# Performance work log

Hardware: AMD Instinct MI355X
Metric: run time of the kernel (lower is better)

The kernel has to match this reference:

```python
import jax, jax.numpy as jnp
import numpy as np

N_ROLES = 6
EPS = 1e-5

def _ln(x, scale, bias):
    m = jnp.mean(x, axis=-1, keepdims=True)
    v = jnp.var(x, axis=-1, keepdims=True)
    return (x - m) * jax.lax.rsqrt(v + EPS) * scale + bias

def setup_inputs() -> dict:
    key = jax.random.key(0)
    ks = jax.random.split(key, 20)
    T, B, D_OBS, H, A = 32, 1024, 256, 512, 32
    inp = {
        'rnn_states': jax.random.normal(ks[0], (B, H), jnp.float32),
        'obs': jax.random.normal(ks[1], (T, B, D_OBS), jnp.float32),
        'resets': jnp.zeros((T, B), jnp.float32),
        'available_actions': jnp.ones((T, B, A), jnp.float32),
        'role_ids': jax.random.randint(ks[2], (T, B), 0, N_ROLES, jnp.int32),
        # feature norm over obs_dim
        'fn_scale': jnp.ones((D_OBS,), jnp.float32),
        'fn_bias': jnp.zeros((D_OBS,), jnp.float32),
        # base MLP: obs_dim->512->512, each followed by LayerNorm
        'W0': jax.random.normal(ks[3], (D_OBS, H), jnp.float32) * 0.02,
        'b0': jnp.zeros((H,), jnp.float32),
        'ln0_scale': jnp.ones((H,), jnp.float32),
        'ln0_bias': jnp.zeros((H,), jnp.float32),
        'W1': jax.random.normal(ks[4], (H, H), jnp.float32) * 0.02,
        'b1': jnp.zeros((H,), jnp.float32),
        'ln1_scale': jnp.ones((H,), jnp.float32),
        'ln1_bias': jnp.zeros((H,), jnp.float32),
        # per-role routes: obs_dim->128->H (stacked over roles)
        'Wr0': jax.random.normal(ks[5], (N_ROLES, D_OBS, 128), jnp.float32) * 0.02,
        'br0': jnp.zeros((N_ROLES, 128), jnp.float32),
        'Wr1': jax.random.normal(ks[6], (N_ROLES, 128, H), jnp.float32) * 0.02,
        'br1': jnp.zeros((N_ROLES, H), jnp.float32),
        # per-role heads: H->64->32->action_dim (stacked over roles)
        'Wh0': jax.random.normal(ks[7], (N_ROLES, H, 64), jnp.float32) * 0.02,
        'bh0': jnp.zeros((N_ROLES, 64), jnp.float32),
        'Wh1': jax.random.normal(ks[8], (N_ROLES, 64, 32), jnp.float32) * 0.02,
        'bh1': jnp.zeros((N_ROLES, 32), jnp.float32),
        'Wh2': jax.random.normal(ks[9], (N_ROLES, 32, A), jnp.float32) * 0.02,
        'bh2': jnp.zeros((N_ROLES, A), jnp.float32),
    }
    return inp

def _gather_by_role(all_values, role_ids):
    # all_values: (K, T, B, F); role_ids: (T, B) -> (T, B, F)
    idx = role_ids[None, :, :, None].astype(jnp.int32)
    return jnp.take_along_axis(all_values, idx, axis=0)[0]

def reference(rnn_states, obs, resets, available_actions, role_ids,
              fn_scale, fn_bias, W0, b0, ln0_scale, ln0_bias,
              W1, b1, ln1_scale, ln1_bias,
              Wr0, br0, Wr1, br1,
              Wh0, bh0, Wh1, bh1, Wh2, bh2):
    # feature normalization on raw obs
    obs_n = _ln(obs, fn_scale, fn_bias)
    # shared base MLP (relu + LayerNorm after each Dense)
    e = _ln(jax.nn.relu(obs_n @ W0 + b0), ln0_scale, ln0_bias)
    e = _ln(jax.nn.relu(e @ W1 + b1), ln1_scale, ln1_bias)
    # per-role pre-GRU residual routes on (normalized) obs
    r = jax.nn.relu(jnp.einsum('tbi,kih->ktbh', obs_n, Wr0) + br0[:, None, None, :])
    r = jax.nn.relu(jnp.einsum('ktbh,kho->ktbo', r, Wr1) + br1[:, None, None, :])
    e = e + _gather_by_role(r, role_ids)
    # no recurrent policy configured: rnn_states pass through
    # per-role heads -> all logits (K, T, B, A)
    h = jax.nn.relu(jnp.einsum('tbh,khf->ktbf', e, Wh0) + bh0[:, None, None, :])
    h = jax.nn.relu(jnp.einsum('ktbf,kfg->ktbg', h, Wh1) + bh1[:, None, None, :])
    all_logits = jnp.einsum('ktbg,kga->ktba', h, Wh2) + bh2[:, None, None, :]
    logits = _gather_by_role(all_logits, role_ids)
    logits = jnp.where(available_actions > 0.5, logits, jnp.full_like(logits, -1e10))
    return rnn_states, logits
```

## Files before the change

### kernel.cpp

```cpp
#include <hip/hip_runtime.h>
#include <stdint.h>

typedef unsigned short u16;
typedef unsigned int u32;

using bf16x8 = __attribute__((ext_vector_type(8))) short;
using f32x4  = __attribute__((ext_vector_type(4))) float;

#define DEVINL __device__ __forceinline__

DEVINL float b2f(u16 u) { return __builtin_bit_cast(float, (u32)u << 16); }
DEVINL u16 f2b(float f) {
  u32 u = __builtin_bit_cast(u32, f);
  u += 0x7FFFu + ((u >> 16) & 1u);
  return (u16)(u >> 16);
}

DEVINL void gll16(const u16* src, u16* dst) {
  __builtin_amdgcn_global_load_lds(
      (const __attribute__((address_space(1))) void*)(uintptr_t)src,
      (__attribute__((address_space(3))) void*)(uintptr_t)dst, 16, 0, 0);
}

#define MFMA __builtin_amdgcn_mfma_f32_16x16x32_bf16
#define NROLE 6

DEVINL void tp_tile(const float* __restrict__ s, u16* __restrict__ d,
                    int R, int C, int bx, int by, int z)
{
  __shared__ u16 tile[32][33];
  const size_t mstride = (size_t)R * C;
  s += (size_t)z * mstride;
  d += (size_t)z * mstride;
  int r0 = bx * 32, c0 = by * 32;
  int tx = threadIdx.x & 31, ty = threadIdx.x >> 5;
#pragma unroll
  for (int i = 0; i < 32; i += 8)
    tile[ty + i][tx] = f2b(s[(size_t)(r0 + ty + i) * C + (c0 + tx)]);
  __syncthreads();
#pragma unroll
  for (int i = 0; i < 32; i += 8)
    d[(size_t)(c0 + ty + i) * R + (r0 + tx)] = tile[tx][ty + i];
}

__global__ __launch_bounds__(256) void mega0(
    const float* W0, const float* W1, const float* Wr0, const float* Wr1, const float* Wh0,
    u16* W0t, u16* W1t, u16* Wr0t, u16* Wr1t, u16* Wh0t,
    const int* __restrict__ rid, int* __restrict__ blkCnt,
    const float* __restrict__ rnn, float* __restrict__ outRnn)
{
  int b = blockIdx.x;
  const int tid = threadIdx.x;
  if (b < 1152) {
    if (b < 128)      {            tp_tile(W0, W0t, 256, 512, b % 8,  b / 8, 0); }
    else if (b < 384) { b -= 128;  tp_tile(W1, W1t, 512, 512, b % 16, b / 16, 0); }
    else if (b < 576) { b -= 384;  int t = b / 8;  tp_tile(Wr0, Wr0t, 256, 128, b % 8,  t % 4,  t / 4); }
    else if (b < 960) { b -= 576;  int t = b / 4;  tp_tile(Wr1, Wr1t, 128, 512, b % 4,  t % 16, t / 16); }
    else              { b -= 960;  int t = b / 16; tp_tile(Wh0, Wh0t, 512, 64,  b % 16, t % 2,  t / 2); }
  } else if (b < 1280) {
    b -= 1152;
    __shared__ int h[NROLE];
    if (tid < NROLE) h[tid] = 0;
    __syncthreads();
    atomicAdd(&h[rid[b * 256 + tid]], 1);
    __syncthreads();
    if (tid < NROLE) blkCnt[b * NROLE + tid] = h[tid];
  } else {
    b -= 1280;
    const float4* src = (const float4*)rnn;
    float4* dst = (float4*)outRnn;
    int base = (b * 256 + tid) * 4;
#pragma unroll
    for (int i = 0; i < 4; ++i) dst[base + i] = src[base + i];
  }
}

__global__ __launch_bounds__(256, 2) void g0f(
    const float* __restrict__ obs, const float* __restrict__ fn_s,
    const float* __restrict__ fn_b, const u16* __restrict__ W0t,
    const float* __restrict__ b0, const float* __restrict__ ln0sc,
    const float* __restrict__ ln0bi, u16* __restrict__ obs_n,
    u16* __restrict__ C,
    const int* __restrict__ rid, const int* __restrict__ blkCnt,
    int* __restrict__ bucket, int* __restrict__ baseArr, int* __restrict__ cntArr)
{
  __shared__ __align__(16) u16 smem[20480];
  const int tid = threadIdx.x;

  if (blockIdx.x >= 512) {
    const int bx = blockIdx.x - 512;
    int* c = (int*)smem;
    int* preArr = c + 768;
    int* scnt   = c + 776;
    int* sbase  = c + 784;
    int* h      = c + 792;
    for (int i = tid; i < 128 * NROLE; i += 256) c[i] = blkCnt[i];
    if (tid < NROLE) h[tid] = 0;
    __syncthreads();
    if (tid < NROLE) {
      int k = tid, run = 0, pre = 0;
      for (int b = 0; b < 128; ++b) { if (b == bx) pre = run; run += c[b * NROLE + k]; }
      scnt[k] = run; preArr[k] = pre;
    }
    __syncthreads();
    if (tid == 0) {
      int r = 0;
      for (int k = 0; k < NROLE; ++k) { sbase[k] = r; r += scnt[k]; }
    }
    __syncthreads();
    if (bx == 0 && tid < NROLE) { baseArr[tid] = sbase[tid]; cntArr[tid] = scnt[tid]; }
    int i = bx * 256 + tid;
    int k = rid[i];
    int pos = atomicAdd(&h[k], 1);
    bucket[sbase[k] + preArr[k] + pos] = i;
    return;
  }

  u16* smA     = smem;
  float* redS  = (float*)&smem[16384];
  float* redSS = (float*)&smem[16896];
  float* prm   = (float*)&smem[17408];
  const int rowBase = blockIdx.x * 64;
  const int lane = tid & 63, wave = tid >> 6;
  const int quad = lane >> 4, lm = lane & 15, l7 = lm & 7;

#pragma unroll
  for (int i = tid; i < 512; i += 256) {
    prm[i] = b0[i]; prm[512 + i] = ln0sc[i]; prm[1024 + i] = ln0bi[i];
  }

  {
    const int r = tid >> 2, q = tid & 3;
    const float* xr = obs + (size_t)(rowBase + r) * 256 + q * 64;
    float x[64];
#pragma unroll
    for (int jj = 0; jj < 16; ++jj)
      *(float4*)&x[jj * 4] = *(const float4*)(xr + jj * 4);
    float s = 0.f, s2 = 0.f;
#pragma unroll
    for (int p = 0; p < 64; ++p) { s += x[p]; s2 += x[p] * x[p]; }
    s  += __shfl_xor(s, 1, 64);  s  += __shfl_xor(s, 2, 64);
    s2 += __shfl_xor(s2, 1, 64); s2 += __shfl_xor(s2, 2, 64);
    float m = s * (1.f / 256.f);
    float var = s2 * (1.f / 256.f) - m * m;
    float inv = rsqrtf(var + 1e-5f);
    const float* fs = fn_s + q * 64;
    const float* fb = fn_b + q * 64;
    u16* og = obs_n + (size_t)(rowBase + r) * 256 + q * 64;
#pragma unroll
    for (int j = 0; j < 8; ++j) {
      float4 fs0 = *(const float4*)(fs + j * 8);
      float4 fs1 = *(const float4*)(fs + j * 8 + 4);
      float4 fb0 = *(const float4*)(fb + j * 8);
      float4 fb1 = *(const float4*)(fb + j * 8 + 4);
      u16 yy[8] __attribute__((aligned(16)));
      yy[0] = f2b((x[j*8+0] - m) * inv * fs0.x + fb0.x);
      yy[1] = f2b((x[j*8+1] - m) * inv * fs0.y + fb0.y);
      yy[2] = f2b((x[j*8+2] - m) * inv * fs0.z + fb0.z);
      yy[3] = f2b((x[j*8+3] - m) * inv * fs0.w + fb0.w);
      yy[4] = f2b((x[j*8+4] - m) * inv * fs1.x + fb1.x);
      yy[5] = f2b((x[j*8+5] - m) * inv * fs1.y + fb1.y);
      yy[6] = f2b((x[j*8+6] - m) * inv * fs1.z + fb1.z);
      yy[7] = f2b((x[j*8+7] - m) * inv * fs1.w + fb1.w);
      int cch = q * 8 + j;
      *(uint4*)&smA[r * 256 + ((cch ^ (r & 7)) * 8)] = *(uint4*)yy;
      *(uint4*)(og + j * 8) = *(uint4*)yy;
    }
  }

  const int wn = wave * 128;
  u32 bOff[8];
#pragma unroll
  for (int j = 0; j < 8; ++j)
    bOff[j] = (u32)(wn + j * 16 + lm) * 256u + (u32)(quad * 8);
  f32x4 acc[4][8] = {};
  bf16x8 bR[2][8];
#pragma unroll
  for (int p = 0; p < 2; ++p)
#pragma unroll
    for (int j = 0; j < 8; ++j)
      bR[p][j] = *(const bf16x8*)(W0t + bOff[j] + p * 32);
  __syncthreads();

#pragma unroll
  for (int g = 0; g < 8; ++g) {
    bf16x8 cur[8];
#pragma unroll
    for (int j = 0; j < 8; ++j) cur[j] = bR[g & 1][j];
    if (g + 2 < 8) {
#pragma unroll
      for (int j = 0; j < 8; ++j)
        bR[g & 1][j] = *(const bf16x8*)(W0t + bOff[j] + (g + 2) * 32);
    }
    const int kc = g * 4;
    bf16x8 af[4];
#pragma unroll
    for (int i2 = 0; i2 < 4; ++i2)
      af[i2] = *(const bf16x8*)&smA[(i2 * 16 + lm) * 256 + (((quad + kc) ^ l7) * 8)];
#pragma unroll
    for (int i2 = 0; i2 < 4; ++i2)
#pragma unroll
      for (int j = 0; j < 8; ++j)
        acc[i2][j] = MFMA(af[i2], cur[j], acc[i2][j], 0, 0, 0);
  }

#pragma unroll
  for (int i2 = 0; i2 < 4; ++i2) {
#pragma unroll
    for (int r2 = 0; r2 < 4; ++r2) {
      float s = 0.f, ss = 0.f;
#pragma unroll
      for (int j = 0; j < 8; ++j) {
        float v = fmaxf(acc[i2][j][r2] + prm[wn + j * 16 + lm], 0.f);
        acc[i2][j][r2] = v;
        s += v; ss += v * v;
      }
#pragma unroll
      for (int o = 1; o < 16; o <<= 1) { s += __shfl_xor(s, o, 64); ss += __shfl_xor(ss, o, 64); }
      if (lm == 0) {
        int rowL = i2 * 16 + quad * 4 + r2;
        redS[rowL * 4 + wave] = s;
        redSS[rowL * 4 + wave] = ss;
      }
    }
  }
  __syncthreads();
#pragma unroll
  for (int i2 = 0; i2 < 4; ++i2) {
#pragma unroll
    for (int r2 = 0; r2 < 4; ++r2) {
      int rowL = i2 * 16 + quad * 4 + r2;
      float ts  = redS[rowL * 4 + 0] + redS[rowL * 4 + 1] + redS[rowL * 4 + 2] + redS[rowL * 4 + 3];
      float tss = redSS[rowL * 4 + 0] + redSS[rowL * 4 + 1] + redSS[rowL * 4 + 2] + redSS[rowL * 4 + 3];
      float m = ts * (1.f / 512.f);
      float var = tss * (1.f / 512.f) - m * m;
      float inv = rsqrtf(var + 1e-5f);
      size_t base = (size_t)(rowBase + rowL) * 512;
#pragma unroll
      for (int j = 0; j < 8; ++j) {
        int col = wn + j * 16 + lm;
        float y = (acc[i2][j][r2] - m) * inv * prm[512 + col] + prm[1024 + col];
        C[base + col] = f2b(y);
      }
    }
  }
}

template <int K>
__global__ __launch_bounds__(256, 2) void gemm_ln(
    const u16* __restrict__ A, const u16* __restrict__ Bt,
    const float* __restrict__ bias, const float* __restrict__ lnsc,
    const float* __restrict__ lnbi, u16* __restrict__ C)
{
  constexpr int BK = 128, NI = K / BK, NC = K / 32;
  __shared__ __align__(16) u16 As[2][64 * BK];
  __shared__ float redS[64][4];
  __shared__ float redSS[64][4];
  __shared__ float prm[1536];
  const int tid = threadIdx.x;
  const int rowBase = blockIdx.x * 64;
  const int lane = tid & 63, wave = tid >> 6;
#pragma unroll
  for (int i = tid; i < 512; i += 256) {
    prm[i] = bias[i]; prm[512 + i] = lnsc[i]; prm[1024 + i] = lnbi[i];
  }
  u32 aOff[4];
#pragma unroll
  for (int r = 0; r < 4; ++r) {
    int row = r * 16 + (tid >> 4);
    int chunk = tid & 15;
    aOff[r] = (u32)(rowBase + row) * (u32)K + (u32)((chunk ^ (row & 7)) * 8);
  }
  const int quad = lane >> 4, lm = lane & 15, l7 = lm & 7;
  const int wn = wave * 128;
  u32 bOff[8];
#pragma unroll
  for (int j = 0; j < 8; ++j)
    bOff[j] = (u32)(wn + j * 16 + lm) * (u32)K + (u32)(quad * 8);

  f32x4 acc[4][8] = {};

#pragma unroll
  for (int r = 0; r < 4; ++r)
    gll16(A + aOff[r], &As[0][r * 2048 + wave * 512]);
  bf16x8 bP[8];
#pragma unroll
  for (int j = 0; j < 8; ++j)
    bP[j] = *(const bf16x8*)(Bt + bOff[j]);
  __syncthreads();

  for (int i = 0; i < NI; ++i) {
    const u16* Ab = As[i & 1];
    if (i + 1 < NI) {
#pragma unroll
      for (int r = 0; r < 4; ++r)
        gll16(A + aOff[r] + (i + 1) * BK, &As[(i + 1) & 1][r * 2048 + wave * 512]);
    }
#pragma unroll
    for (int c = 0; c < 4; ++c) {
      const int g = i * 4 + c;
      bf16x8 bN[8];
      if (g + 1 < NC) {
#pragma unroll
        for (int j = 0; j < 8; ++j)
          bN[j] = *(const bf16x8*)(Bt + bOff[j] + (g + 1) * 32);
      }
      const int kc = c * 4;
      bf16x8 af[4];
#pragma unroll
      for (int i2 = 0; i2 < 4; ++i2)
        af[i2] = *(const bf16x8*)&Ab[(i2 * 16 + lm) * BK + (((quad + kc) ^ l7) * 8)];
#pragma unroll
      for (int i2 = 0; i2 < 4; ++i2)
#pragma unroll
        for (int j = 0; j < 8; ++j)
          acc[i2][j] = MFMA(af[i2], bP[j], acc[i2][j], 0, 0, 0);
      if (g + 1 < NC) {
#pragma unroll
        for (int j = 0; j < 8; ++j) bP[j] = bN[j];
      }
    }
    __syncthreads();
  }

#pragma unroll
  for (int i2 = 0; i2 < 4; ++i2) {
#pragma unroll
    for (int r2 = 0; r2 < 4; ++r2) {
      float s = 0.f, ss = 0.f;
#pragma unroll
      for (int j = 0; j < 8; ++j) {
        float v = fmaxf(acc[i2][j][r2] + prm[wn + j * 16 + lm], 0.f);
        acc[i2][j][r2] = v;
        s += v; ss += v * v;
      }
#pragma unroll
      for (int o = 1; o < 16; o <<= 1) { s += __shfl_xor(s, o, 64); ss += __shfl_xor(ss, o, 64); }
      if (lm == 0) {
        int rowL = i2 * 16 + quad * 4 + r2;
        redS[rowL][wave] = s;
        redSS[rowL][wave] = ss;
      }
    }
  }
  __syncthreads();
#pragma unroll
  for (int i2 = 0; i2 < 4; ++i2) {
#pragma unroll
    for (int r2 = 0; r2 < 4; ++r2) {
      int rowL = i2 * 16 + quad * 4 + r2;
      float ts  = redS[rowL][0] + redS[rowL][1] + redS[rowL][2] + redS[rowL][3];
      float tss = redSS[rowL][0] + redSS[rowL][1] + redSS[rowL][2] + redSS[rowL][3];
      float m = ts * (1.f / 512.f);
      float var = tss * (1.f / 512.f) - m * m;
      float inv = rsqrtf(var + 1e-5f);
      size_t base = (size_t)(rowBase + rowL) * 512;
#pragma unroll
      for (int j = 0; j < 8; ++j) {
        int col = wn + j * 16 + lm;
        float y = (acc[i2][j][r2] - m) * inv * prm[512 + col] + prm[1024 + col];
        C[base + col] = f2b(y);
      }
    }
  }
}

__global__ __launch_bounds__(256, 4) void route_head(
    const u16* __restrict__ obs_n, const u16* __restrict__ e,
    const u16* __restrict__ Wr0t, const float* __restrict__ br0,
    const u16* __restrict__ Wr1t, const float* __restrict__ br1,
    const u16* __restrict__ Wh0t, const float* __restrict__ bh0,
    const float* __restrict__ Wh1, const float* __restrict__ bh1,
    const float* __restrict__ Wh2, const float* __restrict__ bh2,
    const float* __restrict__ avail,
    const int* __restrict__ bucket, const int* __restrict__ baseArr,
    const int* __restrict__ cntArr, float* __restrict__ outLogits)
{
  __shared__ __align__(16) u16 sm[20480];
  const int tid = threadIdx.x;

  int cA0, cA1, cA2, cA3, cA4, cA5, bA0, bA1, bA2, bA3, bA4, bA5;
  {
    int4 ca = *(const int4*)cntArr;  int2 cb = *(const int2*)(cntArr + 4);
    int4 ba = *(const int4*)baseArr; int2 bb = *(const int2*)(baseArr + 4);
    cA0 = ca.x; cA1 = ca.y; cA2 = ca.z; cA3 = ca.w; cA4 = cb.x; cA5 = cb.y;
    bA0 = ba.x; bA1 = ba.y; bA2 = ba.z; bA3 = ba.w; bA4 = bb.x; bA5 = bb.y;
  }
  int role = -1, rem = blockIdx.x, cnt = 0, roleBase = 0;
#define TRY_ROLE(k, ck, bk)                                        \
  if (role < 0) {                                                  \
    int tiles = ((ck) + 31) >> 5;                                  \
    if (rem < tiles) { role = (k); cnt = (ck); roleBase = (bk); }  \
    else rem -= tiles;                                             \
  }
  TRY_ROLE(0, cA0, bA0) TRY_ROLE(1, cA1, bA1) TRY_ROLE(2, cA2, bA2)
  TRY_ROLE(3, cA3, bA3) TRY_ROLE(4, cA4, bA4) TRY_ROLE(5, cA5, bA5)
#undef TRY_ROLE
  if (role < 0) return;
  const int limit = cnt;
  const int rowBase = rem * 32;

  const int lane = tid & 63, wave = tid >> 6;
  const int quad = lane >> 4, lm = lane & 15, l7 = lm & 7;

#pragma unroll
  for (int r = 0; r < 8; ++r) {
    int lrow = r * 4 + wave;
    int i = rowBase + lrow;
    if (i >= limit) i = rowBase;
    int grow = bucket[roleBase + i];
    int chunk = tid & 63;
    int sw = (chunk & 56) | ((chunk ^ lrow) & 7);
    gll16(e + (u32)grow * 512u + (u32)(sw * 8), &sm[r * 2048 + wave * 512]);
  }

  int growA0, growA1;
  {
    int i0 = rowBase + lm;        if (i0 >= limit) i0 = rowBase;
    int i1 = rowBase + 16 + lm;   if (i1 >= limit) i1 = rowBase;
    growA0 = bucket[roleBase + i0];
    growA1 = bucket[roleBase + i1];
  }
  const u16* Ag0 = obs_n + (size_t)growA0 * 256;
  const u16* Ag1 = obs_n + (size_t)growA1 * 256;

  const int wn0 = wave * 32;
  const u16* B0 = Wr0t + (size_t)role * 128 * 256;
  f32x4 acc0[2][2] = {};
  bf16x8 b0R[2][2];
#pragma unroll
  for (int p = 0; p < 2; ++p)
#pragma unroll
    for (int j = 0; j < 2; ++j)
      b0R[p][j] = *(const bf16x8*)(B0 + (u32)(wn0 + j * 16 + lm) * 256u + (u32)(quad * 8 + p * 32));
  bf16x8 aR[4][2];
#pragma unroll
  for (int p = 0; p < 4; ++p) {
    aR[p][0] = *(const bf16x8*)(Ag0 + (u32)(quad * 8 + p * 32));
    aR[p][1] = *(const bf16x8*)(Ag1 + (u32)(quad * 8 + p * 32));
  }
  float bias0[2] = { br0[role * 128 + wn0 + lm], br0[role * 128 + wn0 + 16 + lm] };
#pragma unroll
  for (int it = 0; it < 8; ++it) {
    bf16x8 a0 = aR[it & 3][0], a1 = aR[it & 3][1];
    bf16x8 cur0 = b0R[it & 1][0], cur1 = b0R[it & 1][1];
    if (it + 2 < 8) {
#pragma unroll
      for (int j = 0; j < 2; ++j)
        b0R[it & 1][j] = *(const bf16x8*)(B0 + (u32)(wn0 + j * 16 + lm) * 256u + (u32)(quad * 8 + (it + 2) * 32));
    }
    if (it + 4 < 8) {
      aR[it & 3][0] = *(const bf16x8*)(Ag0 + (u32)(quad * 8 + (it + 4) * 32));
      aR[it & 3][1] = *(const bf16x8*)(Ag1 + (u32)(quad * 8 + (it + 4) * 32));
    }
    acc0[0][0] = MFMA(a0, cur0, acc0[0][0], 0, 0, 0);
    acc0[0][1] = MFMA(a0, cur1, acc0[0][1], 0, 0, 0);
    acc0[1][0] = MFMA(a1, cur0, acc0[1][0], 0, 0, 0);
    acc0[1][1] = MFMA(a1, cur1, acc0[1][1], 0, 0, 0);
  }
  u16* r1 = sm + 16384;
#pragma unroll
  for (int i2 = 0; i2 < 2; ++i2) {
#pragma unroll
    for (int r2 = 0; r2 < 4; ++r2) {
      int row = i2 * 16 + quad * 4 + r2;
#pragma unroll
      for (int j = 0; j < 2; ++j) {
        int col = wn0 + j * 16 + lm;
        float v = fmaxf(acc0[i2][j][r2] + bias0[j], 0.f);
        r1[row * 128 + (((col >> 3) ^ (row & 7)) * 8) + (col & 7)] = f2b(v);
      }
    }
  }
  __syncthreads();

  const int wn1 = wave * 128;
  const u16* B1 = Wr1t + (size_t)role * 512 * 128;
#pragma unroll
  for (int h = 0; h < 2; ++h) {
    const int wnh = wn1 + h * 64;
    float b1v[4];
#pragma unroll
    for (int j = 0; j < 4; ++j) b1v[j] = br1[role * 512 + wnh + j * 16 + lm];
    f32x4 acc1[2][4] = {};
    bf16x8 b1P[4];
#pragma unroll
    for (int j = 0; j < 4; ++j)
      b1P[j] = *(const bf16x8*)(B1 + (u32)(wnh + j * 16 + lm) * 128u + (u32)(quad * 8));
#pragma unroll
    for (int kk = 0; kk < 128; kk += 32) {
      bf16x8 b1N[4];
      if (kk + 32 < 128) {
#pragma unroll
        for (int j = 0; j < 4; ++j)
          b1N[j] = *(const bf16x8*)(B1 + (u32)(wnh + j * 16 + lm) * 128u + (u32)(quad * 8 + kk + 32));
      }
      const int kc = kk >> 3;
      bf16x8 af[2];
#pragma unroll
      for (int i2 = 0; i2 < 2; ++i2)
        af[i2] = *(const bf16x8*)&r1[(i2 * 16 + lm) * 128 + (((quad + kc) ^ l7) * 8)];
#pragma unroll
      for (int i2 = 0; i2 < 2; ++i2)
#pragma unroll
        for (int j = 0; j < 4; ++j)
          acc1[i2][j] = MFMA(af[i2], b1P[j], acc1[i2][j], 0, 0, 0);
      if (kk + 32 < 128) {
#pragma unroll
        for (int j = 0; j < 4; ++j) b1P[j] = b1N[j];
      }
    }
#pragma unroll
    for (int i2 = 0; i2 < 2; ++i2) {
#pragma unroll
      for (int r2 = 0; r2 < 4; ++r2) {
        int row = i2 * 16 + quad * 4 + r2;
#pragma unroll
        for (int j = 0; j < 4; ++j) {
          int col = wnh + j * 16 + lm;
          int addr = row * 512 + (((col >> 3) ^ (row & 7)) * 8) + (col & 7);
          float v = fmaxf(acc1[i2][j][r2] + b1v[j], 0.f) + b2f(sm[addr]);
          sm[addr] = f2b(v);
        }
      }
    }
  }
  __syncthreads();

  const int wn2 = wave * 16;
  const u16* B2 = Wh0t + (size_t)role * 64 * 512;
  float b2v = bh0[role * 64 + wn2 + lm];
  f32x4 acc2[2] = {};
  bf16x8 b2R[4];
#pragma unroll
  for (int p = 0; p < 4; ++p)
    b2R[p] = *(const bf16x8*)(B2 + (u32)(wn2 + lm) * 512u + (u32)(quad * 8 + p * 32));
#pragma unroll
  for (int it = 0; it < 16; ++it) {
    bf16x8 cur = b2R[it & 3];
    if (it + 4 < 16)
      b2R[it & 3] = *(const bf16x8*)(B2 + (u32)(wn2 + lm) * 512u + (u32)(quad * 8 + (it + 4) * 32));
    const int kc = it * 4;
    bf16x8 af[2];
#pragma unroll
    for (int i2 = 0; i2 < 2; ++i2)
      af[i2] = *(const bf16x8*)&sm[(i2 * 16 + lm) * 512 + (((quad + kc) ^ l7) * 8)];
#pragma unroll
    for (int i2 = 0; i2 < 2; ++i2)
      acc2[i2] = MFMA(af[i2], cur, acc2[i2], 0, 0, 0);
  }
  u16* h0s = sm + 16384;
#pragma unroll
  for (int i2 = 0; i2 < 2; ++i2) {
#pragma unroll
    for (int r2 = 0; r2 < 4; ++r2) {
      int row = i2 * 16 + quad * 4 + r2;
      int col = wn2 + lm;
      h0s[row * 68 + col] = f2b(fmaxf(acc2[i2][r2] + b2v, 0.f));
    }
  }
  __syncthreads();

  {
    float* h1s = (float*)&sm[16384];
    const int r = tid >> 3;
    const int n0 = (tid & 7) * 4;
    const bool valid = (rowBase + r) < limit;
    const float* W1k = Wh1 + (size_t)role * 64 * 32;
    const float* W2k = Wh2 + (size_t)role * 32 * 32;
    float4 a1 = *(const float4*)(bh1 + role * 32 + n0);
#pragma unroll 8
    for (int j = 0; j < 64; ++j) {
      float hj = b2f(h0s[r * 68 + j]);
      float4 wv = *(const float4*)(W1k + j * 32 + n0);
      a1.x += hj * wv.x; a1.y += hj * wv.y; a1.z += hj * wv.z; a1.w += hj * wv.w;
    }
    a1.x = fmaxf(a1.x, 0.f); a1.y = fmaxf(a1.y, 0.f);
    a1.z = fmaxf(a1.z, 0.f); a1.w = fmaxf(a1.w, 0.f);
    __syncthreads();
    h1s[r * 36 + n0 + 0] = a1.x;
    h1s[r * 36 + n0 + 1] = a1.y;
    h1s[r * 36 + n0 + 2] = a1.z;
    h1s[r * 36 + n0 + 3] = a1.w;
    __syncthreads();
    float4 a2 = *(const float4*)(bh2 + role * 32 + n0);
#pragma unroll 8
    for (int n = 0; n < 32; ++n) {
      float hn = h1s[r * 36 + n];
      float4 wv = *(const float4*)(W2k + n * 32 + n0);
      a2.x += hn * wv.x; a2.y += hn * wv.y; a2.z += hn * wv.z; a2.w += hn * wv.w;
    }
    if (valid) {
      int g = bucket[roleBase + rowBase + r];
      float4 av = *(const float4*)(avail + (size_t)g * 32 + n0);
      float4 o;
      o.x = (av.x > 0.5f) ? a2.x : -1e10f;
      o.y = (av.y > 0.5f) ? a2.y : -1e10f;
      o.z = (av.z > 0.5f) ? a2.z : -1e10f;
      o.w = (av.w > 0.5f) ? a2.w : -1e10f;
      *(float4*)(outLogits + (size_t)g * 32 + n0) = o;
    }
  }
}

extern "C" void kernel_launch(void* const* d_in, const int* in_sizes, int n_in,
                              void* d_out, int out_size, void* d_ws, size_t ws_size,
                              hipStream_t stream)
{
  const float* rnn  = (const float*)d_in[0];
  const float* obs  = (const float*)d_in[1];
  const float* avail= (const float*)d_in[3];
  const int*   rid  = (const int*)d_in[4];
  const float* fn_s = (const float*)d_in[5];
  const float* fn_b = (const float*)d_in[6];
  const float* W0   = (const float*)d_in[7];
  const float* b0   = (const float*)d_in[8];
  const float* ln0s = (const float*)d_in[9];
  const float* ln0b = (const float*)d_in[10];
  const float* W1   = (const float*)d_in[11];
  const float* b1   = (const float*)d_in[12];
  const float* ln1s = (const float*)d_in[13];
  const float* ln1b = (const float*)d_in[14];
  const float* Wr0  = (const float*)d_in[15];
  const float* br0  = (const float*)d_in[16];
  const float* Wr1  = (const float*)d_in[17];
  const float* br1  = (const float*)d_in[18];
  const float* Wh0  = (const float*)d_in[19];
  const float* bh0  = (const float*)d_in[20];
  const float* Wh1  = (const float*)d_in[21];
  const float* bh1  = (const float*)d_in[22];
  const float* Wh2  = (const float*)d_in[23];
  const float* bh2  = (const float*)d_in[24];

  const int ROWS = 32768;

  char* w = (char*)d_ws;
  auto carve = [&](size_t bytes) { char* p = w; w += (bytes + 255) & ~(size_t)255; return p; };
  u16* obs_n  = (u16*)carve((size_t)ROWS * 256 * 2);
  u16* bufA   = (u16*)carve((size_t)ROWS * 512 * 2);
  u16* bufB   = (u16*)carve((size_t)ROWS * 512 * 2);
  u16* W0t    = (u16*)carve((size_t)512 * 256 * 2);
  u16* W1t    = (u16*)carve((size_t)512 * 512 * 2);
  u16* Wr0t   = (u16*)carve((size_t)6 * 128 * 256 * 2);
  u16* Wr1t   = (u16*)carve((size_t)6 * 512 * 128 * 2);
  u16* Wh0t   = (u16*)carve((size_t)6 * 64 * 512 * 2);
  int* bucket = (int*)carve((size_t)ROWS * 4);
  int* blkCnt = (int*)carve((size_t)128 * NROLE * 4);
  int* baseArr= (int*)carve(256);
  int* cntArr = (int*)carve(256);

  float* outLogits = (float*)d_out + (size_t)1024 * 512;

  mega0<<<1408, 256, 0, stream>>>(W0, W1, Wr0, Wr1, Wh0, W0t, W1t, Wr0t, Wr1t, Wh0t,
                                  rid, blkCnt, rnn, (float*)d_out);

  g0f<<<640, 256, 0, stream>>>(obs, fn_s, fn_b, W0t, b0, ln0s, ln0b,
                               obs_n, bufA, rid, blkCnt, bucket, baseArr, cntArr);

  gemm_ln<512><<<512, 256, 0, stream>>>(bufA, W1t, b1, ln1s, ln1b, bufB);

  route_head<<<1029, 256, 0, stream>>>(obs_n, bufB, Wr0t, br0, Wr1t, br1, Wh0t, bh0,
                                       Wh1, bh1, Wh2, bh2, avail,
                                       bucket, baseArr, cntArr, outLogits);
}
```

Measured before the change: 271.1 us.

## Fuse base MLP layer-1 GEMM+LayerNorm into the layer-0 kernel via LDS

The second base-MLP GEMM with its LayerNorm is merged into the first-layer kernel. The LayerNorm-0 output is written to a swizzled 64x512 bf16 tile in shared memory and consumed directly as the A operand for the W1 GEMM. This removes the 32 MB round trip of the intermediate activation through global memory and one kernel launch. In exchange, shared memory per block rises to about 66 KB, which may limit occupancy, and the layer-1 GEMM uses the simpler register-prefetch B path.

```diff
diff --git a/kernel.cpp b/kernel.cpp
--- a/kernel.cpp
+++ b/kernel.cpp
@@ -75,16 +75,18 @@
   }
 }
 
-__global__ __launch_bounds__(256, 2) void g0f(
+__global__ __launch_bounds__(256, 2) void base2(
     const float* __restrict__ obs, const float* __restrict__ fn_s,
     const float* __restrict__ fn_b, const u16* __restrict__ W0t,
     const float* __restrict__ b0, const float* __restrict__ ln0sc,
-    const float* __restrict__ ln0bi, u16* __restrict__ obs_n,
+    const float* __restrict__ ln0bi, const u16* __restrict__ W1t,
+    const float* __restrict__ b1, const float* __restrict__ ln1sc,
+    const float* __restrict__ ln1bi, u16* __restrict__ obs_n,
     u16* __restrict__ C,
     const int* __restrict__ rid, const int* __restrict__ blkCnt,
     int* __restrict__ bucket, int* __restrict__ baseArr, int* __restrict__ cntArr)
 {
-  __shared__ __align__(16) u16 smem[20480];
+  __shared__ __align__(16) u16 smem[33792];
   const int tid = threadIdx.x;
 
   if (blockIdx.x >= 512) {
@@ -116,18 +118,12 @@
     return;
   }
 
-  u16* smA     = smem;
-  float* redS  = (float*)&smem[16384];
-  float* redSS = (float*)&smem[16896];
-  float* prm   = (float*)&smem[17408];
+  float* redS  = (float*)&smem[32768];
+  float* redSS = redS + 256;
   const int rowBase = blockIdx.x * 64;
   const int lane = tid & 63, wave = tid >> 6;
   const int quad = lane >> 4, lm = lane & 15, l7 = lm & 7;
-
-#pragma unroll
-  for (int i = tid; i < 512; i += 256) {
-    prm[i] = b0[i]; prm[512 + i] = ln0sc[i]; prm[1024 + i] = ln0bi[i];
-  }
+  const int wn = wave * 128;
 
   {
     const int r = tid >> 2, q = tid & 3;
@@ -163,23 +159,22 @@
       yy[6] = f2b((x[j*8+6] - m) * inv * fs1.z + fb1.z);
       yy[7] = f2b((x[j*8+7] - m) * inv * fs1.w + fb1.w);
       int cch = q * 8 + j;
-      *(uint4*)&smA[r * 256 + ((cch ^ (r & 7)) * 8)] = *(uint4*)yy;
+      *(uint4*)&smem[r * 256 + ((cch ^ (r & 7)) * 8)] = *(uint4*)yy;
       *(uint4*)(og + j * 8) = *(uint4*)yy;
     }
   }
 
-  const int wn = wave * 128;
-  u32 bOff[8];
+  u32 bOff0[8];
 #pragma unroll
   for (int j = 0; j < 8; ++j)
-    bOff[j] = (u32)(wn + j * 16 + lm) * 256u + (u32)(quad * 8);
+    bOff0[j] = (u32)(wn + j * 16 + lm) * 256u + (u32)(quad * 8);
   f32x4 acc[4][8] = {};
   bf16x8 bR[2][8];
 #pragma unroll
   for (int p = 0; p < 2; ++p)
 #pragma unroll
     for (int j = 0; j < 8; ++j)
-      bR[p][j] = *(const bf16x8*)(W0t + bOff[j] + p * 32);
+      bR[p][j] = *(const bf16x8*)(W0t + bOff0[j] + p * 32);
   __syncthreads();
 
 #pragma unroll
@@ -190,13 +185,13 @@
     if (g + 2 < 8) {
 #pragma unroll
       for (int j = 0; j < 8; ++j)
-        bR[g & 1][j] = *(const bf16x8*)(W0t + bOff[j] + (g + 2) * 32);
+        bR[g & 1][j] = *(const bf16x8*)(W0t + bOff0[j] + (g + 2) * 32);
     }
     const int kc = g * 4;
     bf16x8 af[4];
 #pragma unroll
     for (int i2 = 0; i2 < 4; ++i2)
-      af[i2] = *(const bf16x8*)&smA[(i2 * 16 + lm) * 256 + (((quad + kc) ^ l7) * 8)];
+      af[i2] = *(const bf16x8*)&smem[(i2 * 16 + lm) * 256 + (((quad + kc) ^ l7) * 8)];
 #pragma unroll
     for (int i2 = 0; i2 < 4; ++i2)
 #pragma unroll
@@ -204,162 +199,148 @@
         acc[i2][j] = MFMA(af[i2], cur[j], acc[i2][j], 0, 0, 0);
   }
 
-#pragma unroll
-  for (int i2 = 0; i2 < 4; ++i2) {
-#pragma unroll
-    for (int r2 = 0; r2 < 4; ++r2) {
-      float s = 0.f, ss = 0.f;
-#pragma unroll
-      for (int j = 0; j < 8; ++j) {
-        float v = fmaxf(acc[i2][j][r2] + prm[wn + j * 16 + lm], 0.f);
-        acc[i2][j][r2] = v;
-        s += v; ss += v * v;
-      }
-#pragma unroll
-      for (int o = 1; o < 16; o <<= 1) { s += __shfl_xor(s, o, 64); ss += __shfl_xor(ss, o, 64); }
-      if (lm == 0) {
-        int rowL = i2 * 16 + quad * 4 + r2;
-        redS[rowL * 4 + wave] = s;
-        redSS[rowL * 4 + wave] = ss;
-      }
-    }
-  }
-  __syncthreads();
-#pragma unroll
-  for (int i2 = 0; i2 < 4; ++i2) {
-#pragma unroll
-    for (int r2 = 0; r2 < 4; ++r2) {
-      int rowL = i2 * 16 + quad * 4 + r2;
-      float ts  = redS[rowL * 4 + 0] + redS[rowL * 4 + 1] + redS[rowL * 4 + 2] + redS[rowL * 4 + 3];
-      float tss = redSS[rowL * 4 + 0] + redSS[rowL * 4 + 1] + redSS[rowL * 4 + 2] + redSS[rowL * 4 + 3];
-      float m = ts * (1.f / 512.f);
-      float var = tss * (1.f / 512.f) - m * m;
-      float inv = rsqrtf(var + 1e-5f);
-      size_t base = (size_t)(rowBase + rowL) * 512;
-#pragma unroll
-      for (int j = 0; j < 8; ++j) {
-        int col = wn + j * 16 + lm;
-        float y = (acc[i2][j][r2] - m) * inv * prm[512 + col] + prm[1024 + col];
-        C[base + col] = f2b(y);
-      }
-    }
-  }
-}
-
-template <int K>
-__global__ __launch_bounds__(256, 2) void gemm_ln(
-    const u16* __restrict__ A, const u16* __restrict__ Bt,
-    const float* __restrict__ bias, const float* __restrict__ lnsc,
-    const float* __restrict__ lnbi, u16* __restrict__ C)
-{
-  constexpr int BK = 128, NI = K / BK, NC = K / 32;
-  __shared__ __align__(16) u16 As[2][64 * BK];
-  __shared__ float redS[64][4];
-  __shared__ float redSS[64][4];
-  __shared__ float prm[1536];
-  const int tid = threadIdx.x;
-  const int rowBase = blockIdx.x * 64;
-  const int lane = tid & 63, wave = tid >> 6;
-#pragma unroll
-  for (int i = tid; i < 512; i += 256) {
-    prm[i] = bias[i]; prm[512 + i] = lnsc[i]; prm[1024 + i] = lnbi[i];
-  }
-  u32 aOff[4];
-#pragma unroll
-  for (int r = 0; r < 4; ++r) {
-    int row = r * 16 + (tid >> 4);
-    int chunk = tid & 15;
-    aOff[r] = (u32)(rowBase + row) * (u32)K + (u32)((chunk ^ (row & 7)) * 8);
-  }
-  const int quad = lane >> 4, lm = lane & 15, l7 = lm & 7;
-  const int wn = wave * 128;
-  u32 bOff[8];
+  {
+    float b0v[8];
+#pragma unroll
+    for (int j = 0; j < 8; ++j) b0v[j] = b0[wn + j * 16 + lm];
+#pragma unroll
+    for (int i2 = 0; i2 < 4; ++i2) {
+#pragma unroll
+      for (int r2 = 0; r2 < 4; ++r2) {
+        float s = 0.f, ss = 0.f;
+#pragma unroll
+        for (int j = 0; j < 8; ++j) {
+          float v = fmaxf(acc[i2][j][r2] + b0v[j], 0.f);
+          acc[i2][j][r2] = v;
+          s += v; ss += v * v;
+        }
+#pragma unroll
+        for (int o = 1; o < 16; o <<= 1) { s += __shfl_xor(s, o, 64); ss += __shfl_xor(ss, o, 64); }
+        if (lm == 0) {
+          int row = i2 * 16 + quad * 4 + r2;
+          redS[row * 4 + wave] = s;
+          redSS[row * 4 + wave] = ss;
+        }
+      }
+    }
+  }
+  __syncthreads();
+
+  {
+    float s0v[8], s0b[8];
+#pragma unroll
+    for (int j = 0; j < 8; ++j) {
+      s0v[j] = ln0sc[wn + j * 16 + lm];
+      s0b[j] = ln0bi[wn + j * 16 + lm];
+    }
+#pragma unroll
+    for (int i2 = 0; i2 < 4; ++i2) {
+#pragma unroll
+      for (int r2 = 0; r2 < 4; ++r2) {
+        int row = i2 * 16 + quad * 4 + r2;
+        float ts  = redS[row * 4 + 0] + redS[row * 4 + 1] + redS[row * 4 + 2] + redS[row * 4 + 3];
+        float tss = redSS[row * 4 + 0] + redSS[row * 4 + 1] + redSS[row * 4 + 2] + redSS[row * 4 + 3];
+        float m = ts * (1.f / 512.f);
+        float var = tss * (1.f / 512.f) - m * m;
+        float inv = rsqrtf(var + 1e-5f);
+#pragma unroll
+        for (int j = 0; j < 8; ++j) {
+          int col = wn + j * 16 + lm;
+          float y = (acc[i2][j][r2] - m) * inv * s0v[j] + s0b[j];
+          smem[row * 512 + (((col >> 3) ^ (row & 7)) * 8) + (col & 7)] = f2b(y);
+        }
+      }
+    }
+  }
+  u32 bOff1[8];
 #pragma unroll
   for (int j = 0; j < 8; ++j)
-    bOff[j] = (u32)(wn + j * 16 + lm) * (u32)K + (u32)(quad * 8);
-
-  f32x4 acc[4][8] = {};
-
-#pragma unroll
-  for (int r = 0; r < 4; ++r)
-    gll16(A + aOff[r], &As[0][r * 2048 + wave * 512]);
-  bf16x8 bP[8];
-#pragma unroll
-  for (int j = 0; j < 8; ++j)
-    bP[j] = *(const bf16x8*)(Bt + bOff[j]);
-  __syncthreads();
-
-  for (int i = 0; i < NI; ++i) {
-    const u16* Ab = As[i & 1];
-    if (i + 1 < NI) {
-#pragma unroll
-      for (int r = 0; r < 4; ++r)
-        gll16(A + aOff[r] + (i + 1) * BK, &As[(i + 1) & 1][r * 2048 + wave * 512]);
-    }
-#pragma unroll
-    for (int c = 0; c < 4; ++c) {
-      const int g = i * 4 + c;
-      bf16x8 bN[8];
-      if (g + 1 < NC) {
-#pragma unroll
-        for (int j = 0; j < 8; ++j)
-          bN[j] = *(const bf16x8*)(Bt + bOff[j] + (g + 1) * 32);
-      }
-      const int kc = c * 4;
-      bf16x8 af[4];
-#pragma unroll
-      for (int i2 = 0; i2 < 4; ++i2)
-        af[i2] = *(const bf16x8*)&Ab[(i2 * 16 + lm) * BK + (((quad + kc) ^ l7) * 8)];
-#pragma unroll
-      for (int i2 = 0; i2 < 4; ++i2)
-#pragma unroll
-        for (int j = 0; j < 8; ++j)
-          acc[i2][j] = MFMA(af[i2], bP[j], acc[i2][j], 0, 0, 0);
-      if (g + 1 < NC) {
-#pragma unroll
-        for (int j = 0; j < 8; ++j) bP[j] = bN[j];
-      }
-    }
-    __syncthreads();
-  }
-
-#pragma unroll
-  for (int i2 = 0; i2 < 4; ++i2) {
-#pragma unroll
-    for (int r2 = 0; r2 < 4; ++r2) {
-      float s = 0.f, ss = 0.f;
-#pragma unroll
-      for (int j = 0; j < 8; ++j) {
-        float v = fmaxf(acc[i2][j][r2] + prm[wn + j * 16 + lm], 0.f);
-        acc[i2][j][r2] = v;
-        s += v; ss += v * v;
-      }
-#pragma unroll
-      for (int o = 1; o < 16; o <<= 1) { s += __shfl_xor(s, o, 64); ss += __shfl_xor(ss, o, 64); }
-      if (lm == 0) {
-        int rowL = i2 * 16 + quad * 4 + r2;
-        redS[rowL][wave] = s;
-        redSS[rowL][wave] = ss;
-      }
-    }
-  }
-  __syncthreads();
-#pragma unroll
-  for (int i2 = 0; i2 < 4; ++i2) {
-#pragma unroll
-    for (int r2 = 0; r2 < 4; ++r2) {
-      int rowL = i2 * 16 + quad * 4 + r2;
-      float ts  = redS[rowL][0] + redS[rowL][1] + redS[rowL][2] + redS[rowL][3];
-      float tss = redSS[rowL][0] + redSS[rowL][1] + redSS[rowL][2] + redSS[rowL][3];
-      float m = ts * (1.f / 512.f);
-      float var = tss * (1.f / 512.f) - m * m;
-      float inv = rsqrtf(var + 1e-5f);
-      size_t base = (size_t)(rowBase + rowL) * 512;
-#pragma unroll
-      for (int j = 0; j < 8; ++j) {
-        int col = wn + j * 16 + lm;
-        float y = (acc[i2][j][r2] - m) * inv * prm[512 + col] + prm[1024 + col];
-        C[base + col] = f2b(y);
+    bOff1[j] = (u32)(wn + j * 16 + lm) * 512u + (u32)(quad * 8);
+#pragma unroll
+  for (int p = 0; p < 2; ++p)
+#pragma unroll
+    for (int j = 0; j < 8; ++j)
+      bR[p][j] = *(const bf16x8*)(W1t + bOff1[j] + p * 32);
+  __syncthreads();
+
+#pragma unroll
+  for (int i2 = 0; i2 < 4; ++i2)
+#pragma unroll
+    for (int j = 0; j < 8; ++j)
+      acc[i2][j] = (f32x4){0.f, 0.f, 0.f, 0.f};
+#pragma unroll
+  for (int g = 0; g < 16; ++g) {
+    bf16x8 cur[8];
+#pragma unroll
+    for (int j = 0; j < 8; ++j) cur[j] = bR[g & 1][j];
+    if (g + 2 < 16) {
+#pragma unroll
+      for (int j = 0; j < 8; ++j)
+        bR[g & 1][j] = *(const bf16x8*)(W1t + bOff1[j] + (g + 2) * 32);
+    }
+    const int kc = g * 4;
+    bf16x8 af[4];
+#pragma unroll
+    for (int i2 = 0; i2 < 4; ++i2)
+      af[i2] = *(const bf16x8*)&smem[(i2 * 16 + lm) * 512 + (((quad + kc) ^ l7) * 8)];
+#pragma unroll
+    for (int i2 = 0; i2 < 4; ++i2)
+#pragma unroll
+      for (int j = 0; j < 8; ++j)
+        acc[i2][j] = MFMA(af[i2], cur[j], acc[i2][j], 0, 0, 0);
+  }
+
+  {
+    float b1v[8];
+#pragma unroll
+    for (int j = 0; j < 8; ++j) b1v[j] = b1[wn + j * 16 + lm];
+#pragma unroll
+    for (int i2 = 0; i2 < 4; ++i2) {
+#pragma unroll
+      for (int r2 = 0; r2 < 4; ++r2) {
+        float s = 0.f, ss = 0.f;
+#pragma unroll
+        for (int j = 0; j < 8; ++j) {
+          float v = fmaxf(acc[i2][j][r2] + b1v[j], 0.f);
+          acc[i2][j][r2] = v;
+          s += v; ss += v * v;
+        }
+#pragma unroll
+        for (int o = 1; o < 16; o <<= 1) { s += __shfl_xor(s, o, 64); ss += __shfl_xor(ss, o, 64); }
+        if (lm == 0) {
+          int row = i2 * 16 + quad * 4 + r2;
+          redS[row * 4 + wave] = s;
+          redSS[row * 4 + wave] = ss;
+        }
+      }
+    }
+  }
+  __syncthreads();
+
+  {
+    float s1v[8], s1b[8];
+#pragma unroll
+    for (int j = 0; j < 8; ++j) {
+      s1v[j] = ln1sc[wn + j * 16 + lm];
+      s1b[j] = ln1bi[wn + j * 16 + lm];
+    }
+#pragma unroll
+    for (int i2 = 0; i2 < 4; ++i2) {
+#pragma unroll
+      for (int r2 = 0; r2 < 4; ++r2) {
+        int row = i2 * 16 + quad * 4 + r2;
+        float ts  = redS[row * 4 + 0] + redS[row * 4 + 1] + redS[row * 4 + 2] + redS[row * 4 + 3];
+        float tss = redSS[row * 4 + 0] + redSS[row * 4 + 1] + redSS[row * 4 + 2] + redSS[row * 4 + 3];
+        float m = ts * (1.f / 512.f);
+        float var = tss * (1.f / 512.f) - m * m;
+        float inv = rsqrtf(var + 1e-5f);
+        size_t base = (size_t)(rowBase + row) * 512;
+#pragma unroll
+        for (int j = 0; j < 8; ++j) {
+          int col = wn + j * 16 + lm;
+          float y = (acc[i2][j][r2] - m) * inv * s1v[j] + s1b[j];
+          C[base + col] = f2b(y);
+        }
       }
     }
   }
@@ -637,7 +618,6 @@
   char* w = (char*)d_ws;
   auto carve = [&](size_t bytes) { char* p = w; w += (bytes + 255) & ~(size_t)255; return p; };
   u16* obs_n  = (u16*)carve((size_t)ROWS * 256 * 2);
-  u16* bufA   = (u16*)carve((size_t)ROWS * 512 * 2);
   u16* bufB   = (u16*)carve((size_t)ROWS * 512 * 2);
   u16* W0t    = (u16*)carve((size_t)512 * 256 * 2);
   u16* W1t    = (u16*)carve((size_t)512 * 512 * 2);
@@ -654,10 +634,9 @@
   mega0<<<1408, 256, 0, stream>>>(W0, W1, Wr0, Wr1, Wh0, W0t, W1t, Wr0t, Wr1t, Wh0t,
                                   rid, blkCnt, rnn, (float*)d_out);
 
-  g0f<<<640, 256, 0, stream>>>(obs, fn_s, fn_b, W0t, b0, ln0s, ln0b,
-                               obs_n, bufA, rid, blkCnt, bucket, baseArr, cntArr);
-
-  gemm_ln<512><<<512, 256, 0, stream>>>(bufA, W1t, b1, ln1s, ln1b, bufB);
+  base2<<<640, 256, 0, stream>>>(obs, fn_s, fn_b, W0t, b0, ln0s, ln0b,
+                                 W1t, b1, ln1s, ln1b, obs_n, bufB,
+                                 rid, blkCnt, bucket, baseArr, cntArr);
 
   route_head<<<1029, 256, 0, stream>>>(obs_n, bufB, Wr0t, br0, Wr1t, br1, Wh0t, bh0,
                                        Wh1, bh1, Wh2, bh2, avail,
```

Result: faster. 263.9 us (-2.6%).
